# Optimization experiments

Measured on AMD Instinct MI355X. Metric: run time of the kernel, lower is better.

Reference implementation:

```python
import jax, jax.numpy as jnp
import numpy as np

N = 50000          # num_nodes
E = 500000         # num_edges
EMB = 50           # embedding_dim
HID = 64           # hidden_dim (per head, conv1)
OUT = 50           # out_dim (conv2, heads=1)
EDIM = 28          # edge_feature_dim
H = 4              # heads (conv1)
NEG_SLOPE = 0.2    # GATv2 leaky_relu slope
EPS_SM = 1e-16     # PyG softmax eps
EPS_LN = 1e-5      # PyG LayerNorm eps


def setup_inputs() -> dict:
    key = jax.random.key(0)
    ks = jax.random.split(key, 24)
    rn = lambda k, shape, s=0.1: jax.random.normal(k, shape, jnp.float32) * s
    return {
        "x": jax.random.randint(ks[0], (N,), 0, N),
        "edge_index": jax.random.randint(ks[1], (2, E), 0, N),
        "edge_attr": rn(ks[2], (E, EDIM), 1.0),
        "emb": rn(ks[3], (N, EMB), 1.0),
        # conv1 (GATv2Conv: lin_l/lin_r with bias, lin_edge no bias, att [H,C], out bias)
        "Wl1": rn(ks[4], (EMB, H * HID)), "bl1": jnp.zeros((H * HID,), jnp.float32),
        "Wr1": rn(ks[5], (EMB, H * HID)), "br1": jnp.zeros((H * HID,), jnp.float32),
        "We1": rn(ks[6], (EDIM, H * HID)),
        "att1": rn(ks[7], (H, HID)),
        "bias1": jnp.zeros((H * HID,), jnp.float32),
        "ln1_w": jnp.ones((H * HID,), jnp.float32), "ln1_b": jnp.zeros((H * HID,), jnp.float32),
        # conv2 (heads=1)
        "Wl2": rn(ks[8], (H * HID, OUT)), "bl2": jnp.zeros((OUT,), jnp.float32),
        "Wr2": rn(ks[9], (H * HID, OUT)), "br2": jnp.zeros((OUT,), jnp.float32),
        "We2": rn(ks[10], (EDIM, OUT)),
        "att2": rn(ks[11], (1, OUT)),
        "bias2": jnp.zeros((OUT,), jnp.float32),
        "ln2_w": jnp.ones((OUT,), jnp.float32), "ln2_b": jnp.zeros((OUT,), jnp.float32),
    }


def gatv2(h, src, dst, ea, Wl, bl, Wr, br, We, att, bias, heads, C):
    n = h.shape[0]
    xl = (h @ Wl + bl).reshape(n, heads, C)   # source transform [N,H,C]
    xr = (h @ Wr + br).reshape(n, heads, C)   # dest transform   [N,H,C]
    xe = (ea @ We).reshape(-1, heads, C)      # edge transform   [E,H,C]
    m = jax.nn.leaky_relu(xl[src] + xr[dst] + xe, NEG_SLOPE)  # [E,H,C]
    logits = jnp.einsum('ehc,hc->eh', m, att)                  # [E,H]
    # edge-softmax over incoming edges of each destination node
    amax = jax.ops.segment_max(logits, dst, num_segments=n)    # [N,H]
    ex = jnp.exp(logits - amax[dst])
    denom = jax.ops.segment_sum(ex, dst, num_segments=n)
    alpha = ex / (denom[dst] + EPS_SM)                         # [E,H]
    out = jax.ops.segment_sum(xl[src] * alpha[..., None], dst, num_segments=n)  # [N,H,C]
    return out.reshape(n, heads * C) + bias


def graph_layernorm(x, w, b):
    # PyG LayerNorm (default mode='graph', batch=None): scalar mean/std over whole tensor
    xc = x - x.mean()
    return xc / (xc.std() + EPS_LN) * w + b


def reference(x, edge_index, edge_attr, emb,
              Wl1, bl1, Wr1, br1, We1, att1, bias1, ln1_w, ln1_b,
              Wl2, bl2, Wr2, br2, We2, att2, bias2, ln2_w, ln2_b):
    src, dst = edge_index[0], edge_index[1]
    h = emb[x]                                                  # [N,EMB]
    h = gatv2(h, src, dst, edge_attr, Wl1, bl1, Wr1, br1, We1, att1, bias1, H, HID)
    h = jax.nn.relu(graph_layernorm(h, ln1_w, ln1_b))
    # dropout p=0.5 is identity in eval mode
    h = gatv2(h, src, dst, edge_attr, Wl2, bl2, Wr2, br2, We2, att2, bias2, 1, OUT)
    return graph_layernorm(h, ln2_w, ln2_b)
```

## Files before the change

kernel.cpp:

```cpp
#include <hip/hip_runtime.h>

#define N_NODES 50000
#define N_EDGES 500000
#define EMB 50
#define HID 64
#define OUTD 50
#define EDIM 28
#define HEADS 4
#define F1 256
#define NEG 0.2f
#define EPS_SM 1e-16f
#define EPS_LN 1e-5f
#define LOG2E 1.4426950408889634f
#define SCAN_B 196

typedef unsigned short u16;
typedef unsigned int u32;
typedef _Float16 hf;
typedef hf h2 __attribute__((ext_vector_type(2)));
typedef hf hf8 __attribute__((ext_vector_type(8)));
typedef float f4 __attribute__((ext_vector_type(4)));
typedef short s8v __attribute__((ext_vector_type(8)));

__device__ __forceinline__ float b2f(u16 u) { return __uint_as_float(((u32)u) << 16); }
__device__ __forceinline__ u16 f2b(float f) {
    u32 u = __float_as_uint(f);
    u32 r = (u + 0x7FFFu + ((u >> 16) & 1u)) >> 16;
    return (u16)r;
}
__device__ __forceinline__ h2 uq(u32 u) { return __builtin_bit_cast(h2, u); }
__device__ __forceinline__ u32 hpack(float a, float b) {
    h2 p = {(hf)a, (hf)b};
    return __builtin_bit_cast(u32, p);
}
__device__ __forceinline__ float lrelu(float x) { return x > 0.f ? x : NEG * x; }

__global__ void k_init(int* __restrict__ cnt, int* __restrict__ cursor, float* __restrict__ S,
                       const float* __restrict__ a, u32* __restrict__ o,
                       const float* __restrict__ We1, const float* __restrict__ We2,
                       u32* __restrict__ Weh1, u32* __restrict__ Weh2,
                       const float* __restrict__ att1, const float* __restrict__ att2,
                       float* __restrict__ atts1, float* __restrict__ atts2,
                       const float* __restrict__ emb, u16* __restrict__ embb) {
    int i = blockIdx.x * blockDim.x + threadIdx.x;
    if (i < N_NODES) cnt[i] = 0;
    else if (i < 2 * N_NODES) cursor[i - N_NODES] = 0;
    else if (i < 2 * N_NODES + 4) S[i - 2 * N_NODES] = 0.f;
    if (i < F1 * 16) {
        int k2 = i >> 8, c = i & 255;
        Weh1[i] = (k2 < 14) ? hpack(We1[(2 * k2) * F1 + c], We1[(2 * k2 + 1) * F1 + c]) : 0u;
    } else if (i < F1 * 16 + 64 * 16) {
        int j = i - F1 * 16;
        int k2 = j >> 6, c = j & 63;
        Weh2[j] = (k2 < 14 && c < OUTD) ? hpack(We2[(2 * k2) * OUTD + c], We2[(2 * k2 + 1) * OUTD + c]) : 0u;
    } else {
        int ja = i - (F1 * 16 + 64 * 16);
        if (ja < 256) atts1[ja] = att1[ja] * LOG2E;
        else if (ja < 320) {
            int c = ja - 256;
            atts2[c] = (c < OUTD) ? att2[c] * LOG2E : 0.f;
        }
    }
    if (i < N_NODES * 64) {
        int node = i >> 6, k = i & 63;
        embb[i] = (k < EMB) ? f2b(emb[(size_t)node * EMB + k]) : (u16)0;
    }
    if (i < N_EDGES * 8) {
        int e = i >> 3, part = i & 7;
        if (part < 7) {
            float4 v = *(const float4*)(a + (size_t)e * EDIM + part * 4);
            *(uint2*)(o + (size_t)e * 16 + part * 2) = make_uint2(hpack(v.x, v.y), hpack(v.z, v.w));
        } else {
            *(uint2*)(o + (size_t)e * 16 + 14) = make_uint2(0u, 0u);
        }
    }
}

__global__ void k_packw(const float* __restrict__ Wl1, const float* __restrict__ Wr1,
                        u16* __restrict__ Wlt1, u16* __restrict__ Wrt1,
                        const float* __restrict__ Wl2, const float* __restrict__ Wr2,
                        u16* __restrict__ Wlt2, u16* __restrict__ Wrt2) {
    int i = blockIdx.x * blockDim.x + threadIdx.x;
    if (i < 256 * 64) {
        int c = i >> 6, k = i & 63;
        Wlt1[i] = (k < EMB) ? f2b(Wl1[k * F1 + c]) : (u16)0;
        Wrt1[i] = (k < EMB) ? f2b(Wr1[k * F1 + c]) : (u16)0;
    } else if (i < 2 * 256 * 64) {
        int j = i - 256 * 64;
        int c = j >> 8, k = j & 255;
        Wlt2[j] = (c < OUTD) ? f2b(Wl2[k * OUTD + c]) : (u16)0;
        Wrt2[j] = (c < OUTD) ? f2b(Wr2[k * OUTD + c]) : (u16)0;
    }
}

__global__ void k_hist(const int* __restrict__ dst, int* __restrict__ cnt) {
    int e = blockIdx.x * blockDim.x + threadIdx.x;
    if (e < N_EDGES) atomicAdd(&cnt[dst[e]], 1);
}

__global__ __launch_bounds__(256) void k_scan1(const int* __restrict__ cnt, int* __restrict__ bsum) {
    int i = blockIdx.x * 256 + threadIdx.x;
    int v = (i < N_NODES) ? cnt[i] : 0;
    #pragma unroll
    for (int off = 32; off; off >>= 1) v += __shfl_xor(v, off);
    __shared__ int ws[4];
    if ((threadIdx.x & 63) == 0) ws[threadIdx.x >> 6] = v;
    __syncthreads();
    if (threadIdx.x == 0) bsum[blockIdx.x] = ws[0] + ws[1] + ws[2] + ws[3];
}

__global__ __launch_bounds__(256) void k_scan2(int* __restrict__ bsum) {
    __shared__ int lds[256];
    int tid = threadIdx.x;
    int v = (tid < SCAN_B) ? bsum[tid] : 0;
    lds[tid] = v;
    __syncthreads();
    for (int off = 1; off < 256; off <<= 1) {
        int t = (tid >= off) ? lds[tid - off] : 0;
        __syncthreads();
        lds[tid] += t;
        __syncthreads();
    }
    if (tid < SCAN_B) bsum[tid] = lds[tid] - v;
}

__global__ __launch_bounds__(256) void k_scan3(const int* __restrict__ cnt, const int* __restrict__ bsum,
                                               int* __restrict__ rowptr) {
    __shared__ int lds[256];
    int tid = threadIdx.x;
    int i = blockIdx.x * 256 + tid;
    int v = (i < N_NODES) ? cnt[i] : 0;
    lds[tid] = v;
    __syncthreads();
    for (int off = 1; off < 256; off <<= 1) {
        int t = (tid >= off) ? lds[tid - off] : 0;
        __syncthreads();
        lds[tid] += t;
        __syncthreads();
    }
    int incl = lds[tid];
    int base = bsum[blockIdx.x];
    if (i < N_NODES) rowptr[i] = base + incl - v;
    if (i == N_NODES - 1) rowptr[N_NODES] = base + incl;
}

__global__ void k_scatter(const int* __restrict__ src, const int* __restrict__ dst,
                          const int* __restrict__ rowptr, int* __restrict__ cursor,
                          int2* __restrict__ epk, int* __restrict__ dstc) {
    int e = blockIdx.x * blockDim.x + threadIdx.x;
    if (e >= N_EDGES) return;
    int d = dst[e];
    int pos = atomicAdd(&cursor[d], 1);
    int j = rowptr[d] + pos;
    epk[j] = make_int2(e << 6, src[e]);
    dstc[j] = d;
}

__global__ __launch_bounds__(256) void k_sumpart(const float* __restrict__ P, int n, float* __restrict__ S) {
    float s1 = 0.f, s2 = 0.f;
    int stride = gridDim.x * blockDim.x;
    for (int i = blockIdx.x * blockDim.x + threadIdx.x; i < n; i += stride) {
        s1 += P[2 * i]; s2 += P[2 * i + 1];
    }
    #pragma unroll
    for (int off = 32; off; off >>= 1) { s1 += __shfl_xor(s1, off); s2 += __shfl_xor(s2, off); }
    __shared__ float w1[4], w2[4];
    int w = threadIdx.x >> 6;
    if ((threadIdx.x & 63) == 0) { w1[w] = s1; w2[w] = s2; }
    __syncthreads();
    if (threadIdx.x == 0) {
        atomicAdd(S,     w1[0] + w1[1] + w1[2] + w1[3]);
        atomicAdd(S + 1, w2[0] + w2[1] + w2[2] + w2[3]);
    }
}

__global__ __launch_bounds__(256) void k_node1(
    const int* __restrict__ x, const u16* __restrict__ embb,
    const u16* __restrict__ Wlt, const u16* __restrict__ Wrt,
    const float* __restrict__ bl, const float* __restrict__ br,
    u16* __restrict__ xl, u16* __restrict__ xr)
{
    int w = threadIdx.x >> 6, lane = threadIdx.x & 63;
    int c = lane & 15, kg = lane >> 4;
    s8v bL[4][2], bR[4][2];
    float blv[4], brv[4];
    #pragma unroll
    for (int ct = 0; ct < 4; ct++) {
        int col = (w << 6) + (ct << 4) + c;
        #pragma unroll
        for (int ks = 0; ks < 2; ks++) {
            bL[ct][ks] = *(const s8v*)(Wlt + ((u32)col << 6) + (ks << 5) + (kg << 3));
            bR[ct][ks] = *(const s8v*)(Wrt + ((u32)col << 6) + (ks << 5) + (kg << 3));
        }
        blv[ct] = bl[col];
        brv[ct] = br[col];
    }
    const int NTILES = N_NODES / 16;
    for (int t = blockIdx.x; t < NTILES; t += gridDim.x) {
        int nb = t << 4;
        int xi = x[nb + c];
        const u16* er = embb + ((u32)xi << 6);
        s8v a0 = *(const s8v*)(er + (kg << 3));
        s8v a1 = *(const s8v*)(er + 32 + (kg << 3));
        #pragma unroll
        for (int ct = 0; ct < 4; ct++) {
            int col = (w << 6) + (ct << 4) + c;
            f4 accL = {blv[ct], blv[ct], blv[ct], blv[ct]};
            f4 accR = {brv[ct], brv[ct], brv[ct], brv[ct]};
            accL = __builtin_amdgcn_mfma_f32_16x16x32_bf16(a0, bL[ct][0], accL, 0, 0, 0);
            accL = __builtin_amdgcn_mfma_f32_16x16x32_bf16(a1, bL[ct][1], accL, 0, 0, 0);
            accR = __builtin_amdgcn_mfma_f32_16x16x32_bf16(a0, bR[ct][0], accR, 0, 0, 0);
            accR = __builtin_amdgcn_mfma_f32_16x16x32_bf16(a1, bR[ct][1], accR, 0, 0, 0);
            #pragma unroll
            for (int i = 0; i < 4; i++) {
                int node = nb + (kg << 2) + i;
                xl[((size_t)node << 8) + col] = f2b(accL[i]);
                xr[((size_t)node << 8) + col] = f2b(accR[i]);
            }
        }
    }
}

__global__ __launch_bounds__(256) void k_logits1(
    const int2* __restrict__ epk, const int* __restrict__ dstc,
    const u32* __restrict__ eah, const u16* __restrict__ xl, const u16* __restrict__ xr,
    const u32* __restrict__ Weh, const float* __restrict__ atts,
    float* __restrict__ Lg)
{
    int lane = threadIdx.x & 63;
    int er = lane & 15, grp = lane >> 4;
    hf8 wA[16];
    #pragma unroll
    for (int ct = 0; ct < 16; ct++) {
        uint4 q;
        q.x = Weh[(grp * 4 + 0) * 256 + ct * 16 + er];
        q.y = Weh[(grp * 4 + 1) * 256 + ct * 16 + er];
        q.z = Weh[(grp * 4 + 2) * 256 + ct * 16 + er];
        q.w = Weh[(grp * 4 + 3) * 256 + ct * 16 + er];
        wA[ct] = __builtin_bit_cast(hf8, q);
    }
    int wid = blockIdx.x * 4 + (threadIdx.x >> 6);
    int nw = gridDim.x * 4;
    const int NT = N_EDGES / 16;
    const char* eab = (const char*)eah;
    const f4 zero = {0.f, 0.f, 0.f, 0.f};
    if (wid >= NT) return;
    int2 p = epk[wid * 16 + er];
    int d = dstc[wid * 16 + er];
    hf8 bfrag = *(const hf8*)(eab + (u32)p.x + (grp << 4));
    for (int t = wid; t < NT; t += nw) {
        int tn = t + nw;
        int2 pn; int dn; hf8 bfn;
        if (tn < NT) {
            pn = epk[tn * 16 + er];
            dn = dstc[tn * 16 + er];
            bfn = *(const hf8*)(eab + (u32)pn.x + (grp << 4));
        }
        int j = t * 16 + er;
        const u16* xlp = xl + ((u32)p.y << 8);
        const u16* xrp = xr + ((u32)d << 8);
        float part0 = 0.f, part1 = 0.f, part2 = 0.f, part3 = 0.f;
        #pragma unroll
        for (int ct = 0; ct < 16; ct++) {
            int c0 = ct * 16 + grp * 4;
            f4 z = __builtin_amdgcn_mfma_f32_16x16x32_f16(wA[ct], bfrag, zero, 0, 0, 0);
            uint2 ql = *(const uint2*)(xlp + c0);
            uint2 qr = *(const uint2*)(xrp + c0);
            float4 av = *(const float4*)(atts + c0);
            float z0 = z[0] + __uint_as_float(ql.x << 16)        + __uint_as_float(qr.x << 16);
            float z1 = z[1] + __uint_as_float(ql.x & 0xFFFF0000u) + __uint_as_float(qr.x & 0xFFFF0000u);
            float z2 = z[2] + __uint_as_float(ql.y << 16)        + __uint_as_float(qr.y << 16);
            float z3 = z[3] + __uint_as_float(ql.y & 0xFFFF0000u) + __uint_as_float(qr.y & 0xFFFF0000u);
            float s = av.x * fmaxf(z0, NEG * z0) + av.y * fmaxf(z1, NEG * z1)
                    + av.z * fmaxf(z2, NEG * z2) + av.w * fmaxf(z3, NEG * z3);
            if      (ct < 4)  part0 += s;
            else if (ct < 8)  part1 += s;
            else if (ct < 12) part2 += s;
            else              part3 += s;
        }
        part0 += __shfl_xor(part0, 16); part0 += __shfl_xor(part0, 32);
        part1 += __shfl_xor(part1, 16); part1 += __shfl_xor(part1, 32);
        part2 += __shfl_xor(part2, 16); part2 += __shfl_xor(part2, 32);
        part3 += __shfl_xor(part3, 16); part3 += __shfl_xor(part3, 32);
        float v01 = (grp & 1) ? part1 : part0;
        float v23 = (grp & 1) ? part3 : part2;
        float v = (grp & 2) ? v23 : v01;
        Lg[((size_t)j << 2) + grp] = v;
        p = pn; d = dn; bfrag = bfn;
    }
}

__global__ __launch_bounds__(256) void k_fused1(
    const int* __restrict__ rowptr, const int2* __restrict__ epk,
    const float* __restrict__ Lg, const u16* __restrict__ xl,
    const float* __restrict__ bias, u16* __restrict__ out, float* __restrict__ Spart)
{
    int node = blockIdx.x;
    int tid = threadIdx.x;
    int h = tid >> 6, lane = tid & 63;
    int beg = rowptr[node], end = rowptr[node + 1];
    float acc = 0.f, dtot = 0.f;
    int j = beg;
    for (; j + 3 < end; j += 4) {
        int2 pA = epk[j], pB = epk[j + 1], pC = epk[j + 2], pD = epk[j + 3];
        float g1 = Lg[((size_t)j << 2) + h];
        float g2 = Lg[((size_t)j << 2) + 4 + h];
        float g3 = Lg[((size_t)j << 2) + 8 + h];
        float g4 = Lg[((size_t)j << 2) + 12 + h];
        float xA = b2f(xl[((u32)pA.y << 8) + tid]);
        float xB = b2f(xl[((u32)pB.y << 8) + tid]);
        float xC = b2f(xl[((u32)pC.y << 8) + tid]);
        float xD = b2f(xl[((u32)pD.y << 8) + tid]);
        float p1 = exp2f(g1), p2 = exp2f(g2), p3 = exp2f(g3), p4 = exp2f(g4);
        acc  += (p1 * xA + p2 * xB) + (p3 * xC + p4 * xD);
        dtot += (p1 + p2) + (p3 + p4);
    }
    for (; j < end; j++) {
        int2 p = epk[j];
        float pe = exp2f(Lg[((size_t)j << 2) + h]);
        float xA = b2f(xl[((u32)p.y << 8) + tid]);
        acc += pe * xA; dtot += pe;
    }
    float o = ((end > beg) ? acc / (dtot + EPS_SM) : 0.f) + bias[tid];
    out[((size_t)node << 8) + tid] = f2b(o);
    float s1 = o, s2 = o * o;
    #pragma unroll
    for (int off = 32; off; off >>= 1) { s1 += __shfl_xor(s1, off); s2 += __shfl_xor(s2, off); }
    __shared__ float ls1[4], ls2[4];
    if (lane == 0) { ls1[h] = s1; ls2[h] = s2; }
    __syncthreads();
    if (tid == 0) {
        Spart[(size_t)node * 2]     = ls1[0] + ls1[1] + ls1[2] + ls1[3];
        Spart[(size_t)node * 2 + 1] = ls2[0] + ls2[1] + ls2[2] + ls2[3];
    }
}

__global__ void k_ln_apply_relu_b(
    u16* v, const float* __restrict__ w, const float* __restrict__ b,
    const float* __restrict__ S, int M, int C)
{
    int i = blockIdx.x * blockDim.x + threadIdx.x;
    if (i >= M) return;
    float mu = S[0] / (float)M;
    float var = S[1] / (float)M - mu * mu;
    float inv = 1.f / (sqrtf(fmaxf(var, 0.f)) + EPS_LN);
    int c = i % C;
    float y = (b2f(v[i]) - mu) * inv * w[c] + b[c];
    v[i] = f2b(fmaxf(y, 0.f));
}

__global__ void k_ln_out(
    const float* __restrict__ v, const float* __restrict__ w, const float* __restrict__ b,
    const float* __restrict__ S, int M, int C, float* __restrict__ out)
{
    int i = blockIdx.x * blockDim.x + threadIdx.x;
    if (i >= M) return;
    float mu = S[0] / (float)M;
    float var = S[1] / (float)M - mu * mu;
    float inv = 1.f / (sqrtf(fmaxf(var, 0.f)) + EPS_LN);
    int c = i % C;
    out[i] = (v[i] - mu) * inv * w[c] + b[c];
}

__global__ __launch_bounds__(256) void k_node2(
    const u16* __restrict__ h, const u16* __restrict__ Wlt, const u16* __restrict__ Wrt,
    const float* __restrict__ bl, const float* __restrict__ br,
    u16* __restrict__ xlb, u16* __restrict__ xrb)
{
    int w = threadIdx.x >> 6, lane = threadIdx.x & 63;
    int c = lane & 15, kg = lane >> 4;
    int col = (w << 4) + c;
    s8v bL[8], bR[8];
    #pragma unroll
    for (int ks = 0; ks < 8; ks++) {
        bL[ks] = *(const s8v*)(Wlt + ((u32)col << 8) + (ks << 5) + (kg << 3));
        bR[ks] = *(const s8v*)(Wrt + ((u32)col << 8) + (ks << 5) + (kg << 3));
    }
    float blv = (col < OUTD) ? bl[col] : 0.f;
    float brv = (col < OUTD) ? br[col] : 0.f;
    const int NTILES = N_NODES / 16;
    for (int t = blockIdx.x; t < NTILES; t += gridDim.x) {
        int nb = t << 4;
        const u16* hrow = h + ((size_t)(nb + c) << 8) + (kg << 3);
        f4 accL = {blv, blv, blv, blv};
        f4 accR = {brv, brv, brv, brv};
        #pragma unroll
        for (int ks = 0; ks < 8; ks++) {
            s8v a = *(const s8v*)(hrow + (ks << 5));
            accL = __builtin_amdgcn_mfma_f32_16x16x32_bf16(a, bL[ks], accL, 0, 0, 0);
            accR = __builtin_amdgcn_mfma_f32_16x16x32_bf16(a, bR[ks], accR, 0, 0, 0);
        }
        #pragma unroll
        for (int i = 0; i < 4; i++) {
            int node = nb + (kg << 2) + i;
            xlb[((u32)node << 6) + col] = f2b(accL[i]);
            xrb[((u32)node << 6) + col] = f2b(accR[i]);
        }
    }
}

__global__ __launch_bounds__(256) void k_logits2(
    const int2* __restrict__ epk, const int* __restrict__ dstc,
    const u32* __restrict__ eah, const u16* __restrict__ xlb, const u16* __restrict__ xrb,
    const u32* __restrict__ Weh, const float* __restrict__ atts,
    float* __restrict__ Lg2)
{
    int lane = threadIdx.x & 63;
    int er = lane & 15, grp = lane >> 4;
    hf8 wA[4];
    #pragma unroll
    for (int ct = 0; ct < 4; ct++) {
        uint4 q;
        q.x = Weh[(grp * 4 + 0) * 64 + ct * 16 + er];
        q.y = Weh[(grp * 4 + 1) * 64 + ct * 16 + er];
        q.z = Weh[(grp * 4 + 2) * 64 + ct * 16 + er];
        q.w = Weh[(grp * 4 + 3) * 64 + ct * 16 + er];
        wA[ct] = __builtin_bit_cast(hf8, q);
    }
    int wid = blockIdx.x * 4 + (threadIdx.x >> 6);
    int nw = gridDim.x * 4;
    const int NT = N_EDGES / 16;
    const char* eab = (const char*)eah;
    const f4 zero = {0.f, 0.f, 0.f, 0.f};
    if (wid >= NT) return;
    int2 p = epk[wid * 16 + er];
    int d = dstc[wid * 16 + er];
    hf8 bfrag = *(const hf8*)(eab + (u32)p.x + (grp << 4));
    for (int t = wid; t < NT; t += nw) {
        int tn = t + nw;
        int2 pn; int dn; hf8 bfn;
        if (tn < NT) {
            pn = epk[tn * 16 + er];
            dn = dstc[tn * 16 + er];
            bfn = *(const hf8*)(eab + (u32)pn.x + (grp << 4));
        }
        int j = t * 16 + er;
        const u16* xlp = xlb + ((u32)p.y << 6);
        const u16* xrp = xrb + ((u32)d << 6);
        float tot = 0.f;
        #pragma unroll
        for (int ct = 0; ct < 4; ct++) {
            int c0 = ct * 16 + grp * 4;
            f4 z = __builtin_amdgcn_mfma_f32_16x16x32_f16(wA[ct], bfrag, zero, 0, 0, 0);
            uint2 ql = *(const uint2*)(xlp + c0);
            uint2 qr = *(const uint2*)(xrp + c0);
            float4 av = *(const float4*)(atts + c0);
            float z0 = z[0] + __uint_as_float(ql.x << 16)        + __uint_as_float(qr.x << 16);
            float z1 = z[1] + __uint_as_float(ql.x & 0xFFFF0000u) + __uint_as_float(qr.x & 0xFFFF0000u);
            float z2 = z[2] + __uint_as_float(ql.y << 16)        + __uint_as_float(qr.y << 16);
            float z3 = z[3] + __uint_as_float(ql.y & 0xFFFF0000u) + __uint_as_float(qr.y & 0xFFFF0000u);
            tot += av.x * fmaxf(z0, NEG * z0) + av.y * fmaxf(z1, NEG * z1)
                 + av.z * fmaxf(z2, NEG * z2) + av.w * fmaxf(z3, NEG * z3);
        }
        tot += __shfl_xor(tot, 16);
        tot += __shfl_xor(tot, 32);
        if (lane < 16) Lg2[j] = tot;
        p = pn; d = dn; bfrag = bfn;
    }
}

__global__ __launch_bounds__(256) void k_fused2(
    const int* __restrict__ rowptr, const int2* __restrict__ epk,
    const float* __restrict__ Lg2, const u16* __restrict__ xlb,
    const float* __restrict__ bias, float* __restrict__ out, float* __restrict__ Spart)
{
    int w = threadIdx.x >> 6, lane = threadIdx.x & 63;
    int node = blockIdx.x * 4 + w;
    bool col = lane < OUTD;
    int beg = rowptr[node], end = rowptr[node + 1];
    float acc = 0.f, dtot = 0.f;
    int j = beg;
    for (; j + 3 < end; j += 4) {
        int2 p0 = epk[j], p1 = epk[j + 1], p2 = epk[j + 2], p3 = epk[j + 3];
        float g0 = Lg2[j], g1 = Lg2[j + 1], g2 = Lg2[j + 2], g3 = Lg2[j + 3];
        float x0 = b2f(xlb[((u32)p0.y << 6) + lane]);
        float x1 = b2f(xlb[((u32)p1.y << 6) + lane]);
        float x2 = b2f(xlb[((u32)p2.y << 6) + lane]);
        float x3 = b2f(xlb[((u32)p3.y << 6) + lane]);
        float e0 = exp2f(g0), e1 = exp2f(g1), e2 = exp2f(g2), e3 = exp2f(g3);
        acc  += (e0 * x0 + e1 * x1) + (e2 * x2 + e3 * x3);
        dtot += (e0 + e1) + (e2 + e3);
    }
    for (; j < end; j++) {
        int2 p = epk[j];
        float e = exp2f(Lg2[j]);
        float xv = b2f(xlb[((u32)p.y << 6) + lane]);
        acc += e * xv; dtot += e;
    }
    float s1 = 0.f, s2 = 0.f;
    if (col) {
        float o = ((end > beg) ? acc / (dtot + EPS_SM) : 0.f) + bias[lane];
        out[(u32)node * OUTD + lane] = o;
        s1 = o; s2 = o * o;
    }
    #pragma unroll
    for (int off = 32; off; off >>= 1) { s1 += __shfl_xor(s1, off); s2 += __shfl_xor(s2, off); }
    __shared__ float ls1[4], ls2[4];
    if (lane == 0) { ls1[w] = s1; ls2[w] = s2; }
    __syncthreads();
    if (threadIdx.x == 0) {
        Spart[(size_t)blockIdx.x * 2]     = ls1[0] + ls1[1] + ls1[2] + ls1[3];
        Spart[(size_t)blockIdx.x * 2 + 1] = ls2[0] + ls2[1] + ls2[2] + ls2[3];
    }
}

extern "C" void kernel_launch(void* const* d_in, const int* in_sizes, int n_in,
                              void* d_out, int out_size, void* d_ws, size_t ws_size,
                              hipStream_t stream)
{
    const int*   x    = (const int*)d_in[0];
    const int*   ei   = (const int*)d_in[1];
    const int*   srcA = ei;
    const int*   dstA = ei + N_EDGES;
    const float* ea   = (const float*)d_in[2];
    const float* emb  = (const float*)d_in[3];
    const float* Wl1  = (const float*)d_in[4];
    const float* bl1  = (const float*)d_in[5];
    const float* Wr1  = (const float*)d_in[6];
    const float* br1  = (const float*)d_in[7];
    const float* We1  = (const float*)d_in[8];
    const float* att1 = (const float*)d_in[9];
    const float* bias1= (const float*)d_in[10];
    const float* ln1w = (const float*)d_in[11];
    const float* ln1b = (const float*)d_in[12];
    const float* Wl2  = (const float*)d_in[13];
    const float* bl2  = (const float*)d_in[14];
    const float* Wr2  = (const float*)d_in[15];
    const float* br2  = (const float*)d_in[16];
    const float* We2  = (const float*)d_in[17];
    const float* att2 = (const float*)d_in[18];
    const float* bias2= (const float*)d_in[19];
    const float* ln2w = (const float*)d_in[20];
    const float* ln2b = (const float*)d_in[21];

    float* W = (float*)d_ws;
    u16*   xl1b    = (u16*)W;
    u16*   xr1b    = (u16*)(W + 6400000);
    u16*   out1b   = (u16*)(W + 12800000);
    u32*   eah     = (u32*)(W + 19200000);
    int2*  epk     = (int2*)(W + 27200000);
    int*   rowptr  = (int*)(W + 28200000);
    int*   cnt     = (int*)(W + 28260000);
    int*   cursor  = (int*)(W + 28310000);
    float* Spart   = W + 28360000;
    float* S       = W + 28460000;
    int*   bsum    = (int*)(W + 28461000);
    u32*   Weh1    = (u32*)(W + 28470000);
    u32*   Weh2    = (u32*)(W + 28480000);
    float* atts1   = W + 28481100;
    float* atts2   = W + 28481600;
    int*   dstc    = (int*)(W + 28482000);
    u16*   Wlt2    = (u16*)(W + 28982000);
    u16*   Wrt2    = (u16*)(W + 28991000);
    float* Lg      = W + 29000000;
    u16*   embb    = (u16*)(W + 29000000);
    u16*   Wlt1    = (u16*)(W + 30600000);
    u16*   Wrt1    = (u16*)(W + 30610000);
    u16*   xl2b    = (u16*)W;
    u16*   xr2b    = (u16*)(W + 1600000);
    float* out2    = W + 3200000;
    float* Lg2     = W + 29000000;
    u16*   h1      = out1b;

    k_init<<<(N_EDGES * 8 + 255) / 256, 256, 0, stream>>>(cnt, cursor, S, ea, eah,
                                                          We1, We2, Weh1, Weh2,
                                                          att1, att2, atts1, atts2,
                                                          emb, embb);
    k_packw<<<128, 256, 0, stream>>>(Wl1, Wr1, Wlt1, Wrt1, Wl2, Wr2, Wlt2, Wrt2);
    k_hist<<<(N_EDGES + 255) / 256, 256, 0, stream>>>(dstA, cnt);
    k_scan1<<<SCAN_B, 256, 0, stream>>>(cnt, bsum);
    k_scan2<<<1, 256, 0, stream>>>(bsum);
    k_scan3<<<SCAN_B, 256, 0, stream>>>(cnt, bsum, rowptr);
    k_scatter<<<(N_EDGES + 255) / 256, 256, 0, stream>>>(srcA, dstA, rowptr, cursor, epk, dstc);

    k_node1<<<1024, 256, 0, stream>>>(x, embb, Wlt1, Wrt1, bl1, br1, xl1b, xr1b);
    k_logits1<<<1024, 256, 0, stream>>>(epk, dstc, eah, xl1b, xr1b, Weh1, atts1, Lg);
    k_fused1<<<N_NODES, 256, 0, stream>>>(rowptr, epk, Lg, xl1b, bias1, out1b, Spart);
    k_sumpart<<<32, 256, 0, stream>>>(Spart, N_NODES, S);
    k_ln_apply_relu_b<<<(N_NODES * F1 + 255) / 256, 256, 0, stream>>>(h1, ln1w, ln1b, S, N_NODES * F1, F1);

    k_node2<<<1024, 256, 0, stream>>>(h1, Wlt2, Wrt2, bl2, br2, xl2b, xr2b);
    k_logits2<<<1024, 256, 0, stream>>>(epk, dstc, eah, xl2b, xr2b, Weh2, atts2, Lg2);
    k_fused2<<<N_NODES / 4, 256, 0, stream>>>(rowptr, epk, Lg2, xl2b, bias2, out2, Spart);
    k_sumpart<<<32, 256, 0, stream>>>(Spart, N_NODES / 4, S + 2);
    k_ln_out<<<(N_NODES * OUTD + 255) / 256, 256, 0, stream>>>(out2, ln2w, ln2b, S + 2, N_NODES * OUTD, OUTD, (float*)d_out);
}
```

Measured before the change: 526.2 us.

## Map one wavefront per node in layer-1 aggregation with 4-channel vector loads

```diff
diff --git a/kernel.cpp b/kernel.cpp
--- a/kernel.cpp
+++ b/kernel.cpp
@@ -295,43 +295,58 @@
     const float* __restrict__ Lg, const u16* __restrict__ xl,
     const float* __restrict__ bias, u16* __restrict__ out, float* __restrict__ Spart)
 {
-    int node = blockIdx.x;
-    int tid = threadIdx.x;
-    int h = tid >> 6, lane = tid & 63;
+    int w = threadIdx.x >> 6, lane = threadIdx.x & 63;
+    int node = blockIdx.x * 4 + w;
+    int h = lane >> 4;
+    int c0 = lane << 2;
     int beg = rowptr[node], end = rowptr[node + 1];
-    float acc = 0.f, dtot = 0.f;
+    float a0 = 0.f, a1 = 0.f, a2 = 0.f, a3 = 0.f, dtot = 0.f;
     int j = beg;
     for (; j + 3 < end; j += 4) {
         int2 pA = epk[j], pB = epk[j + 1], pC = epk[j + 2], pD = epk[j + 3];
-        float g1 = Lg[((size_t)j << 2) + h];
-        float g2 = Lg[((size_t)j << 2) + 4 + h];
-        float g3 = Lg[((size_t)j << 2) + 8 + h];
-        float g4 = Lg[((size_t)j << 2) + 12 + h];
-        float xA = b2f(xl[((u32)pA.y << 8) + tid]);
-        float xB = b2f(xl[((u32)pB.y << 8) + tid]);
-        float xC = b2f(xl[((u32)pC.y << 8) + tid]);
-        float xD = b2f(xl[((u32)pD.y << 8) + tid]);
-        float p1 = exp2f(g1), p2 = exp2f(g2), p3 = exp2f(g3), p4 = exp2f(g4);
-        acc  += (p1 * xA + p2 * xB) + (p3 * xC + p4 * xD);
-        dtot += (p1 + p2) + (p3 + p4);
+        float gA = Lg[((size_t)j << 2) + h];
+        float gB = Lg[((size_t)(j + 1) << 2) + h];
+        float gC = Lg[((size_t)(j + 2) << 2) + h];
+        float gD = Lg[((size_t)(j + 3) << 2) + h];
+        uint2 xA = *(const uint2*)(xl + ((u32)pA.y << 8) + c0);
+        uint2 xB = *(const uint2*)(xl + ((u32)pB.y << 8) + c0);
+        uint2 xC = *(const uint2*)(xl + ((u32)pC.y << 8) + c0);
+        uint2 xD = *(const uint2*)(xl + ((u32)pD.y << 8) + c0);
+        float eA = exp2f(gA), eB = exp2f(gB), eC = exp2f(gC), eD = exp2f(gD);
+        a0 += (eA * b2f((u16)xA.x) + eB * b2f((u16)xB.x)) + (eC * b2f((u16)xC.x) + eD * b2f((u16)xD.x));
+        a1 += (eA * b2f((u16)(xA.x >> 16)) + eB * b2f((u16)(xB.x >> 16)))
+            + (eC * b2f((u16)(xC.x >> 16)) + eD * b2f((u16)(xD.x >> 16)));
+        a2 += (eA * b2f((u16)xA.y) + eB * b2f((u16)xB.y)) + (eC * b2f((u16)xC.y) + eD * b2f((u16)xD.y));
+        a3 += (eA * b2f((u16)(xA.y >> 16)) + eB * b2f((u16)(xB.y >> 16)))
+            + (eC * b2f((u16)(xC.y >> 16)) + eD * b2f((u16)(xD.y >> 16)));
+        dtot += (eA + eB) + (eC + eD);
     }
     for (; j < end; j++) {
         int2 p = epk[j];
-        float pe = exp2f(Lg[((size_t)j << 2) + h]);
-        float xA = b2f(xl[((u32)p.y << 8) + tid]);
-        acc += pe * xA; dtot += pe;
-    }
-    float o = ((end > beg) ? acc / (dtot + EPS_SM) : 0.f) + bias[tid];
-    out[((size_t)node << 8) + tid] = f2b(o);
-    float s1 = o, s2 = o * o;
+        float e = exp2f(Lg[((size_t)j << 2) + h]);
+        uint2 xv = *(const uint2*)(xl + ((u32)p.y << 8) + c0);
+        a0 += e * b2f((u16)xv.x);
+        a1 += e * b2f((u16)(xv.x >> 16));
+        a2 += e * b2f((u16)xv.y);
+        a3 += e * b2f((u16)(xv.y >> 16));
+        dtot += e;
+    }
+    float inv = (end > beg) ? 1.f / (dtot + EPS_SM) : 0.f;
+    float4 bv = *(const float4*)(bias + c0);
+    float o0 = a0 * inv + bv.x;
+    float o1 = a1 * inv + bv.y;
+    float o2 = a2 * inv + bv.z;
+    float o3 = a3 * inv + bv.w;
+    u32 lo = (u32)f2b(o0) | ((u32)f2b(o1) << 16);
+    u32 hi = (u32)f2b(o2) | ((u32)f2b(o3) << 16);
+    *(uint2*)(out + ((size_t)node << 8) + c0) = make_uint2(lo, hi);
+    float s1 = (o0 + o1) + (o2 + o3);
+    float s2 = (o0 * o0 + o1 * o1) + (o2 * o2 + o3 * o3);
     #pragma unroll
     for (int off = 32; off; off >>= 1) { s1 += __shfl_xor(s1, off); s2 += __shfl_xor(s2, off); }
-    __shared__ float ls1[4], ls2[4];
-    if (lane == 0) { ls1[h] = s1; ls2[h] = s2; }
-    __syncthreads();
-    if (tid == 0) {
-        Spart[(size_t)node * 2]     = ls1[0] + ls1[1] + ls1[2] + ls1[3];
-        Spart[(size_t)node * 2 + 1] = ls2[0] + ls2[1] + ls2[2] + ls2[3];
+    if (lane == 0) {
+        Spart[(size_t)node * 2]     = s1;
+        Spart[(size_t)node * 2 + 1] = s2;
     }
 }
 
@@ -575,7 +590,7 @@
 
     k_node1<<<1024, 256, 0, stream>>>(x, embb, Wlt1, Wrt1, bl1, br1, xl1b, xr1b);
     k_logits1<<<1024, 256, 0, stream>>>(epk, dstc, eah, xl1b, xr1b, Weh1, atts1, Lg);
-    k_fused1<<<N_NODES, 256, 0, stream>>>(rowptr, epk, Lg, xl1b, bias1, out1b, Spart);
+    k_fused1<<<N_NODES / 4, 256, 0, stream>>>(rowptr, epk, Lg, xl1b, bias1, out1b, Spart);
     k_sumpart<<<32, 256, 0, stream>>>(Spart, N_NODES, S);
     k_ln_apply_relu_b<<<(N_NODES * F1 + 255) / 256, 256, 0, stream>>>(h1, ln1w, ln1b, S, N_NODES * F1, F1);
 
```

Result: faster. 488.6 us (-7.1%).
